# Kernel optimization log

Measured on AMD Instinct MI355X. Metric: run time of the kernel, lower is better.

Reference implementation:

```python
import jax, jax.numpy as jnp
import numpy as np

DIM = 1024
NUM_HEADS = 16
HEAD_DIM = DIM // NUM_HEADS  # 64
WINDOW = 256
SCALE = HEAD_DIM ** -0.5


def setup_inputs() -> dict:
    key = jax.random.key(0)
    ks = jax.random.split(key, 5)
    B, L = 4, 4096
    x = jax.random.normal(ks[0], (B, L, DIM), dtype=jnp.float32)
    # Linear weights stored torch-style as (out_features, in_features)
    q_w = jax.random.normal(ks[1], (DIM, DIM), dtype=jnp.float32) * (DIM ** -0.5)
    kv_w = jax.random.normal(ks[2], (2 * HEAD_DIM, DIM), dtype=jnp.float32) * (DIM ** -0.5)
    proj_w = jax.random.normal(ks[3], (DIM, DIM), dtype=jnp.float32) * (DIM ** -0.5)
    proj_b = jax.random.normal(ks[4], (DIM,), dtype=jnp.float32) * 0.01
    return {"x": x, "q_w": q_w, "kv_w": kv_w, "proj_w": proj_w, "proj_b": proj_b}


def reference(x, q_w, kv_w, proj_w, proj_b):
    B, L, D = x.shape
    H, hd, ws = NUM_HEADS, HEAD_DIM, WINDOW
    # MQA projections
    q = x @ q_w.T                                  # (B, L, D)
    kv = x @ kv_w.T                                # (B, L, 2*hd)
    k, v = kv[..., :hd], kv[..., hd:]              # (B, L, hd) single KV head
    q = q.reshape(B, L, H, hd).transpose(0, 2, 1, 3)  # (B, H, L, hd)
    # Pad sequence to a multiple of the window size (static at trace time)
    pad = (ws - L % ws) % ws
    Lp = L + pad
    if pad > 0:
        q = jnp.pad(q, ((0, 0), (0, 0), (0, pad), (0, 0)))
        k = jnp.pad(k, ((0, 0), (0, pad), (0, 0)))
        v = jnp.pad(v, ((0, 0), (0, pad), (0, 0)))
    n = Lp // ws
    qb = q.reshape(B, H, n, ws, hd)                # (B, H, n, w, d)
    kb = k.reshape(B, n, ws, hd)                   # (B, n, w, d) broadcast over heads
    vb = v.reshape(B, n, ws, hd)
    # Dense per-window attention with MQA-aware KV broadcast (no expand)
    attn = jnp.einsum('bhnwd,bnud->bhnwu', qb, kb) * SCALE
    attn = jax.nn.softmax(attn, axis=-1)
    out = jnp.einsum('bhnwu,bnud->bhnwd', attn, vb)  # (B, H, n, w, d)
    out = out.reshape(B, H, Lp, hd)[:, :, :L, :]
    out = out.transpose(0, 2, 1, 3).reshape(B, L, D)  # b h l d -> b l (h d)
    return out @ proj_w.T + proj_b
```

## Files before the change

### kernel.cpp

```cpp
#include <hip/hip_runtime.h>

typedef short bf16x8 __attribute__((ext_vector_type(8)));
typedef float f32x4 __attribute__((ext_vector_type(4)));

#define QSCALE 0.18033688011112042f

__device__ __forceinline__ unsigned short f2bf(float x) {
  unsigned int u = __float_as_uint(x);
  u = (u + 0x7FFFu + ((u >> 16) & 1u)) >> 16;
  return (unsigned short)u;
}

__device__ __forceinline__ unsigned pack_rn(float a, float b) {
  unsigned au = __float_as_uint(a) + 0x8000u;
  unsigned bu = __float_as_uint(b) + 0x8000u;
  return (bu & 0xFFFF0000u) | (au >> 16);
}

__device__ __forceinline__ void async16(const void* g, void* l) {
  typedef const __attribute__((address_space(1))) unsigned int* gp_t;
  typedef __attribute__((address_space(3))) unsigned int* lp_t;
  __builtin_amdgcn_global_load_lds((gp_t)g, (lp_t)l, 16, 0, 0);
}

union frag_u { bf16x8 f; unsigned int u[4]; };

__global__ void cast_bf16(const float* __restrict__ in, unsigned short* __restrict__ out, int n4) {
  int i = blockIdx.x * 256 + threadIdx.x;
  if (i >= n4) return;
  float4 v = ((const float4*)in)[i];
  ushort4 o;
  o.x = f2bf(v.x); o.y = f2bf(v.y); o.z = f2bf(v.z); o.w = f2bf(v.w);
  ((ushort4*)out)[i] = o;
}

__global__ void cast_w3(const float* __restrict__ qw, const float* __restrict__ kvw,
                        const float* __restrict__ pw, unsigned short* __restrict__ qwo,
                        unsigned short* __restrict__ kvwo, unsigned short* __restrict__ pwo) {
  int i = blockIdx.x * 256 + threadIdx.x;
  const float* src; unsigned short* dst; int j;
  if (i < 262144)      { src = qw;  dst = qwo;  j = i; }
  else if (i < 294912) { src = kvw; dst = kvwo; j = i - 262144; }
  else                 { src = pw;  dst = pwo;  j = i - 294912; }
  float4 v = ((const float4*)src)[j];
  ushort4 o;
  o.x = f2bf(v.x); o.y = f2bf(v.y); o.z = f2bf(v.z); o.w = f2bf(v.w);
  ((ushort4*)dst)[j] = o;
}

template<int MODE>
__global__ __launch_bounds__(512, 2) void gemm256(
    const unsigned short* __restrict__ A,
    const unsigned short* __restrict__ Bw,
    unsigned short* __restrict__ Cbf,
    float* __restrict__ Cf,
    const float* __restrict__ bias,
    const float oscale,
    int M, int N, int K)
{
  __shared__ unsigned short S[65536];
  const int t = threadIdx.x;
  const int lane = t & 63, wave = t >> 6;
  const int g = lane >> 4, r = lane & 15;
  const int wm = wave >> 2, wn = wave & 3;

  const int nby = N >> 8;
  const int cpx = gridDim.x >> 3;
  const int bid = blockIdx.x;
  const int swz = (bid & 7) * cpx + (bid >> 3);
  const long row0 = (long)(swz / nby) * 256;
  const long col0 = (long)(swz % nby) * 256;

  const int NT = K >> 6;

  auto stage = [&](const unsigned short* gsrc, long grow0, int kcol0, int region) {
#pragma unroll
    for (int i = 0; i < 2; ++i) {
      int o = (i * 512 + t) << 4;
      int row = o >> 7;
      int scol = (o & 127) ^ ((row & 7) << 4);
      async16(gsrc + (grow0 + row) * K + kcol0 + (scol >> 1),
              (char*)S + region + i * 8192 + wave * 1024);
    }
  };
  auto ldA = [&](int bo, int ar, int ks) {
    return *(const bf16x8*)((const char*)S + bo + ar * 128 +
                            ((ks * 64 + g * 16) ^ ((ar & 7) << 4)));
  };
  auto ldB = [&](int bo, int br, int ks) {
    return *(const bf16x8*)((const char*)S + bo + 32768 + br * 128 +
                            ((ks * 64 + g * 16) ^ ((br & 7) << 4)));
  };

  f32x4 acc[8][4] = {};
  bf16x8 aF[4][2], b01[2][2], b23[2][2];

  stage(A,  row0,       0, 0);
  stage(A,  row0 + 128, 0, 16384);
  stage(Bw, col0,       0, 32768);
  stage(Bw, col0 + 128, 0, 32768 + 16384);
  if (NT > 1) {
    stage(Bw, col0,       64, 65536 + 32768);
    stage(Bw, col0 + 128, 64, 65536 + 32768 + 16384);
    asm volatile("s_waitcnt vmcnt(4)" ::: "memory");
  } else {
    asm volatile("s_waitcnt vmcnt(0)" ::: "memory");
  }
  __builtin_amdgcn_s_barrier();

  for (int kt = 0; kt < NT; ++kt) {
    const int bo = (kt & 1) << 16;
    if (kt + 1 < NT) {
      stage(A, row0,       (kt + 1) * 64, bo ^ 65536);
      stage(A, row0 + 128, (kt + 1) * 64, (bo ^ 65536) + 16384);
    }
#pragma unroll
    for (int mf = 0; mf < 4; ++mf) {
      int ar = wm * 128 + mf * 16 + r;
      aF[mf][0] = ldA(bo, ar, 0); aF[mf][1] = ldA(bo, ar, 1);
    }
#pragma unroll
    for (int nf = 0; nf < 2; ++nf) {
      int br = wn * 64 + nf * 16 + r;
      b01[nf][0] = ldB(bo, br, 0); b01[nf][1] = ldB(bo, br, 1);
    }
#pragma unroll
    for (int nf = 0; nf < 2; ++nf) {
      int br = wn * 64 + (nf + 2) * 16 + r;
      b23[nf][0] = ldB(bo, br, 0); b23[nf][1] = ldB(bo, br, 1);
    }
    __builtin_amdgcn_s_setprio(1);
#pragma unroll
    for (int mf = 0; mf < 4; ++mf)
#pragma unroll
      for (int nf = 0; nf < 2; ++nf) {
        acc[mf][nf] = __builtin_amdgcn_mfma_f32_16x16x32_bf16(aF[mf][0], b01[nf][0], acc[mf][nf], 0, 0, 0);
        acc[mf][nf] = __builtin_amdgcn_mfma_f32_16x16x32_bf16(aF[mf][1], b01[nf][1], acc[mf][nf], 0, 0, 0);
        acc[mf][nf + 2] = __builtin_amdgcn_mfma_f32_16x16x32_bf16(aF[mf][0], b23[nf][0], acc[mf][nf + 2], 0, 0, 0);
        acc[mf][nf + 2] = __builtin_amdgcn_mfma_f32_16x16x32_bf16(aF[mf][1], b23[nf][1], acc[mf][nf + 2], 0, 0, 0);
      }
    __builtin_amdgcn_s_setprio(0);
    __builtin_amdgcn_s_barrier();
    if (kt + 2 < NT) {
      stage(Bw, col0,       (kt + 2) * 64, bo + 32768);
      stage(Bw, col0 + 128, (kt + 2) * 64, bo + 32768 + 16384);
    }
#pragma unroll
    for (int mf = 0; mf < 4; ++mf) {
      int ar = wm * 128 + (mf + 4) * 16 + r;
      aF[mf][0] = ldA(bo, ar, 0); aF[mf][1] = ldA(bo, ar, 1);
    }
    __builtin_amdgcn_s_setprio(1);
#pragma unroll
    for (int mf = 0; mf < 4; ++mf)
#pragma unroll
      for (int nf = 0; nf < 2; ++nf) {
        acc[mf + 4][nf] = __builtin_amdgcn_mfma_f32_16x16x32_bf16(aF[mf][0], b01[nf][0], acc[mf + 4][nf], 0, 0, 0);
        acc[mf + 4][nf] = __builtin_amdgcn_mfma_f32_16x16x32_bf16(aF[mf][1], b01[nf][1], acc[mf + 4][nf], 0, 0, 0);
        acc[mf + 4][nf + 2] = __builtin_amdgcn_mfma_f32_16x16x32_bf16(aF[mf][0], b23[nf][0], acc[mf + 4][nf + 2], 0, 0, 0);
        acc[mf + 4][nf + 2] = __builtin_amdgcn_mfma_f32_16x16x32_bf16(aF[mf][1], b23[nf][1], acc[mf + 4][nf + 2], 0, 0, 0);
      }
    __builtin_amdgcn_s_setprio(0);
    if (kt < NT - 2)      asm volatile("s_waitcnt vmcnt(4)" ::: "memory");
    else if (kt < NT - 1) asm volatile("s_waitcnt vmcnt(0)" ::: "memory");
    if (kt < NT - 1) __builtin_amdgcn_s_barrier();
  }

  if (MODE == 0) {
#pragma unroll
    for (int mf = 0; mf < 8; ++mf)
#pragma unroll
      for (int nf = 0; nf < 4; ++nf) {
        long rr = row0 + wm * 128 + mf * 16 + g * 4;
        long cc = col0 + wn * 64 + nf * 16 + r;
#pragma unroll
        for (int i = 0; i < 4; ++i)
          Cbf[(rr + i) * N + cc] = f2bf(acc[mf][nf][i] * oscale);
      }
  } else {
#pragma unroll
    for (int mf = 0; mf < 8; ++mf)
#pragma unroll
      for (int nf = 0; nf < 4; ++nf) {
        long rr = row0 + wm * 128 + mf * 16 + g * 4;
        long cc = col0 + wn * 64 + nf * 16 + r;
        float bb = bias[cc];
#pragma unroll
        for (int i = 0; i < 4; ++i)
          Cf[(rr + i) * N + cc] = acc[mf][nf][i] + bb;
      }
  }
}

__global__ __launch_bounds__(256) void gemm_kv(
    const unsigned short* __restrict__ A,
    const unsigned short* __restrict__ Bw,
    unsigned short* __restrict__ Kout,
    unsigned short* __restrict__ VTout,
    int M, int N, int K)
{
  __shared__ unsigned short As[128 * 64];
  __shared__ unsigned short Bs[128 * 64];
  const int t = threadIdx.x;
  const int lane = t & 63, wave = t >> 6;
  const int g = lane >> 4, r = lane & 15;
  const int wr = wave >> 1, wc = wave & 1;
  const long row0 = (long)blockIdx.x * 128;
  const long col0 = 0;

  f32x4 acc[4][4] = {};

  for (int kt = 0; kt < K; kt += 64) {
    __syncthreads();
#pragma unroll
    for (int i = 0; i < 4; ++i) {
      int o = (i * 256 + t) << 4;
      int arow = o >> 7;
      int scol = (o & 127) ^ ((arow & 7) << 4);
      async16(A + (row0 + arow) * K + kt + (scol >> 1), (char*)As + (i * 4096 + wave * 1024));
    }
#pragma unroll
    for (int i = 0; i < 4; ++i) {
      int o = (i * 256 + t) << 4;
      int brow = o >> 7;
      int scol = (o & 127) ^ ((brow & 7) << 4);
      async16(Bw + (col0 + brow) * K + kt + (scol >> 1), (char*)Bs + (i * 4096 + wave * 1024));
    }
    __syncthreads();
#pragma unroll
    for (int ks = 0; ks < 2; ++ks) {
      bf16x8 af[4], bfr[4];
#pragma unroll
      for (int rf = 0; rf < 4; ++rf) {
        int ar = wr * 64 + rf * 16 + r;
        af[rf] = *(const bf16x8*)((const char*)As + ar * 128 + ((ks * 64 + g * 16) ^ ((ar & 7) << 4)));
      }
#pragma unroll
      for (int cf = 0; cf < 4; ++cf) {
        int br = wc * 64 + cf * 16 + r;
        bfr[cf] = *(const bf16x8*)((const char*)Bs + br * 128 + ((ks * 64 + g * 16) ^ ((br & 7) << 4)));
      }
#pragma unroll
      for (int rf = 0; rf < 4; ++rf)
#pragma unroll
        for (int cf = 0; cf < 4; ++cf)
          acc[rf][cf] = __builtin_amdgcn_mfma_f32_16x16x32_bf16(af[rf], bfr[cf], acc[rf][cf], 0, 0, 0);
    }
  }

  if (wc == 0) {
#pragma unroll
    for (int rf = 0; rf < 4; ++rf)
#pragma unroll
      for (int cf = 0; cf < 4; ++cf) {
        long rr = row0 + wr * 64 + rf * 16 + g * 4;
        int cc = cf * 16 + r;
#pragma unroll
        for (int i = 0; i < 4; ++i)
          Kout[(rr + i) * 64 + cc] = f2bf(acc[rf][cf][i]);
      }
  } else {
#pragma unroll
    for (int rf = 0; rf < 4; ++rf)
#pragma unroll
      for (int cf = 0; cf < 4; ++cf) {
        long tok = row0 + wr * 64 + rf * 16 + g * 4;
        long w16 = tok >> 8;
        int kp = (int)(tok & 255);
        int hd = cf * 16 + r;
        ushort4 pk;
        pk.x = f2bf(acc[rf][cf][0]); pk.y = f2bf(acc[rf][cf][1]);
        pk.z = f2bf(acc[rf][cf][2]); pk.w = f2bf(acc[rf][cf][3]);
        *(ushort4*)(VTout + (w16 * 64 + hd) * 256 + kp) = pk;
      }
  }
}

__global__ __launch_bounds__(512, 2) void attn_win(
    const unsigned short* __restrict__ qb,
    const unsigned short* __restrict__ kb,
    const unsigned short* __restrict__ vt,
    unsigned short* __restrict__ ao)
{
  __shared__ unsigned short Ks[256 * 64];
  __shared__ unsigned short Vs[64 * 256];

  const int blk = blockIdx.x;
  const int hp = blk & 7;
  const int w16 = blk >> 3;
  const long tok0 = (long)w16 * 256;
  const int t = threadIdx.x;
  const int lane = t & 63, wave = t >> 6;
  const int g = lane >> 4, r = lane & 15;
  const int h = hp * 2 + (wave >> 2);
  const int qw = wave & 3;

#pragma unroll
  for (int i = 0; i < 4; ++i) {
    int o = (i * 512 + t) << 4;
    int row = o >> 7;
    int ph = ((row & 3) << 1) | ((row >> 3) & 1);
    int scol = (o & 127) ^ (ph << 4);
    async16(kb + (tok0 + row) * 64 + (scol >> 1), (char*)Ks + i * 8192 + wave * 1024);
  }
  const unsigned short* vbase = vt + (long)w16 * (64 * 256);
#pragma unroll
  for (int i = 0; i < 4; ++i) {
    int o = (i * 512 + t) << 4;
    int hd = o >> 9;
    int scol = (o & 511) ^ ((hd & 7) << 4);
    async16(vbase + (long)hd * 256 + (scol >> 1), (char*)Vs + i * 8192 + wave * 1024);
  }

  bf16x8 qf[4][2];
#pragma unroll
  for (int cq = 0; cq < 4; ++cq)
#pragma unroll
    for (int kh = 0; kh < 2; ++kh)
      qf[cq][kh] = *(const bf16x8*)(qb + (tok0 + qw * 64 + cq * 16 + r) * 1024 + h * 64 + kh * 32 + g * 8);

  f32x4 O[4][4] = {};
  float sp[4] = {0.f, 0.f, 0.f, 0.f};
  const int rsub = 8 * (r >> 2) + (r & 3);
  __syncthreads();

#pragma unroll
  for (int kc = 0; kc < 8; ++kc) {
    f32x4 sc[2][4] = {};
#pragma unroll
    for (int kr = 0; kr < 2; ++kr) {
      int kp = kc * 32 + kr * 4 + rsub;
      int ph = ((kp & 3) << 1) | ((kp >> 3) & 1);
      bf16x8 kf0 = *(const bf16x8*)((const char*)Ks + kp * 128 + ((g * 16) ^ (ph << 4)));
      bf16x8 kf1 = *(const bf16x8*)((const char*)Ks + kp * 128 + ((64 + g * 16) ^ (ph << 4)));
#pragma unroll
      for (int cq = 0; cq < 4; ++cq) {
        sc[kr][cq] = __builtin_amdgcn_mfma_f32_16x16x32_bf16(kf0, qf[cq][0], sc[kr][cq], 0, 0, 0);
        sc[kr][cq] = __builtin_amdgcn_mfma_f32_16x16x32_bf16(kf1, qf[cq][1], sc[kr][cq], 0, 0, 0);
      }
    }
    bf16x8 vf[4];
#pragma unroll
    for (int ch = 0; ch < 4; ++ch) {
      int hd = ch * 16 + r;
      vf[ch] = *(const bf16x8*)((const char*)Vs + hd * 512 + ((kc * 64 + g * 16) ^ ((hd & 7) << 4)));
    }
#pragma unroll
    for (int cq = 0; cq < 4; ++cq) {
#pragma unroll
      for (int kr = 0; kr < 2; ++kr)
#pragma unroll
        for (int i = 0; i < 4; ++i)
          sc[kr][cq][i] = __builtin_amdgcn_exp2f(sc[kr][cq][i]);
      sp[cq] += ((sc[0][cq][0] + sc[0][cq][1]) + (sc[0][cq][2] + sc[0][cq][3])) +
                ((sc[1][cq][0] + sc[1][cq][1]) + (sc[1][cq][2] + sc[1][cq][3]));
    }
#pragma unroll
    for (int rq = 0; rq < 4; ++rq) {
      frag_u pa;
      pa.u[0] = pack_rn(sc[0][rq][0], sc[0][rq][1]);
      pa.u[1] = pack_rn(sc[0][rq][2], sc[0][rq][3]);
      pa.u[2] = pack_rn(sc[1][rq][0], sc[1][rq][1]);
      pa.u[3] = pack_rn(sc[1][rq][2], sc[1][rq][3]);
#pragma unroll
      for (int ch = 0; ch < 4; ++ch)
        O[rq][ch] = __builtin_amdgcn_mfma_f32_16x16x32_bf16(pa.f, vf[ch], O[rq][ch], 0, 0, 0);
    }
  }
  float inv[4];
#pragma unroll
  for (int cq = 0; cq < 4; ++cq) {
    float s = sp[cq];
    s += __shfl_xor(s, 16);
    s += __shfl_xor(s, 32);
    inv[cq] = 1.0f / s;
  }
#pragma unroll
  for (int rq = 0; rq < 4; ++rq)
#pragma unroll
    for (int i = 0; i < 4; ++i) {
      float w = __shfl(inv[rq], g * 4 + i);
      long tokr = tok0 + qw * 64 + rq * 16 + g * 4 + i;
#pragma unroll
      for (int ch = 0; ch < 4; ++ch)
        ao[tokr * 1024 + h * 64 + ch * 16 + r] = f2bf(O[rq][ch][i] * w);
    }
}

extern "C" void kernel_launch(void* const* d_in, const int* in_sizes, int n_in,
                              void* d_out, int out_size, void* d_ws, size_t ws_size,
                              hipStream_t stream) {
  const float* x      = (const float*)d_in[0];
  const float* q_w    = (const float*)d_in[1];
  const float* kv_w   = (const float*)d_in[2];
  const float* proj_w = (const float*)d_in[3];
  const float* proj_b = (const float*)d_in[4];

  char* ws = (char*)d_ws;
  unsigned short* x_bf   = (unsigned short*)(ws + 0);
  unsigned short* q_bf   = (unsigned short*)(ws + 33554432);
  unsigned short* ao_bf  = (unsigned short*)(ws + 67108864);
  unsigned short* qw_bf  = (unsigned short*)(ws + 100663296);
  unsigned short* pw_bf  = (unsigned short*)(ws + 102760448);
  unsigned short* kvw_bf = (unsigned short*)(ws + 104857600);
  unsigned short* k_bf   = (unsigned short*)(ws + 105119744);
  unsigned short* vt_bf  = (unsigned short*)(ws + 107216896);
  if (ws_size < 109314048) return;

  cast_bf16<<<16384, 256, 0, stream>>>(x, x_bf, 4194304);
  cast_w3<<<2176, 256, 0, stream>>>(q_w, kv_w, proj_w, qw_bf, kvw_bf, pw_bf);

  gemm256<0><<<256, 512, 0, stream>>>(x_bf, qw_bf, q_bf, nullptr, nullptr, QSCALE, 16384, 1024, 1024);
  gemm_kv<<<128, 256, 0, stream>>>(x_bf, kvw_bf, k_bf, vt_bf, 16384, 128, 1024);
  attn_win<<<512, 512, 0, stream>>>(q_bf, k_bf, vt_bf, ao_bf);
  gemm256<1><<<256, 512, 0, stream>>>(ao_bf, pw_bf, nullptr, (float*)d_out, proj_b, 1.0f, 16384, 1024, 1024);
}
```

Baseline: 148.5 us.

## Fuse fp32-to-bf16 cast of x into Q and KV projection GEMM loads

Removes the standalone cast kernel for x and has both the Q-projection GEMM and the KV GEMM read fp32 x directly. Each thread loads float4s into registers, packs them to bf16 and writes them swizzled into shared memory, replacing the async global-to-LDS copy for the A operand. This saves a full write and re-read of the 32 MB bf16 copy of x and one launch. In exchange the GEMMs read twice as many A bytes, and x is now read twice in fp32, once per GEMM. The register staging also adds VGPR pressure and extra waitcnt/barrier handling in the pipelined loop.

```diff
diff --git a/kernel.cpp b/kernel.cpp
--- a/kernel.cpp
+++ b/kernel.cpp
@@ -2,6 +2,7 @@
 
 typedef short bf16x8 __attribute__((ext_vector_type(8)));
 typedef float f32x4 __attribute__((ext_vector_type(4)));
+typedef unsigned int u32x4 __attribute__((ext_vector_type(4)));
 
 #define QSCALE 0.18033688011112042f
 
@@ -24,15 +25,6 @@
 }
 
 union frag_u { bf16x8 f; unsigned int u[4]; };
-
-__global__ void cast_bf16(const float* __restrict__ in, unsigned short* __restrict__ out, int n4) {
-  int i = blockIdx.x * 256 + threadIdx.x;
-  if (i >= n4) return;
-  float4 v = ((const float4*)in)[i];
-  ushort4 o;
-  o.x = f2bf(v.x); o.y = f2bf(v.y); o.z = f2bf(v.z); o.w = f2bf(v.w);
-  ((ushort4*)out)[i] = o;
-}
 
 __global__ void cast_w3(const float* __restrict__ qw, const float* __restrict__ kvw,
                         const float* __restrict__ pw, unsigned short* __restrict__ qwo,
@@ -50,7 +42,7 @@
 
 template<int MODE>
 __global__ __launch_bounds__(512, 2) void gemm256(
-    const unsigned short* __restrict__ A,
+    const void* __restrict__ Asrc,
     const unsigned short* __restrict__ Bw,
     unsigned short* __restrict__ Cbf,
     float* __restrict__ Cf,
@@ -73,15 +65,32 @@
 
   const int NT = K >> 6;
 
-  auto stage = [&](const unsigned short* gsrc, long grow0, int kcol0, int region) {
-#pragma unroll
-    for (int i = 0; i < 2; ++i) {
-      int o = (i * 512 + t) << 4;
-      int row = o >> 7;
-      int scol = (o & 127) ^ ((row & 7) << 4);
-      async16(gsrc + (grow0 + row) * K + kcol0 + (scol >> 1),
-              (char*)S + region + i * 8192 + wave * 1024);
-    }
+  const float* Af = (const float*)Asrc;
+  const unsigned short* Ab = (const unsigned short*)Asrc;
+
+  auto stageB = [&](int kt, int region) {
+#pragma unroll
+    for (int h = 0; h < 2; ++h)
+#pragma unroll
+      for (int i = 0; i < 2; ++i) {
+        int o = (i * 512 + t) << 4;
+        int row = o >> 7;
+        int scol = (o & 127) ^ ((row & 7) << 4);
+        async16(Bw + (col0 + h * 128 + row) * K + kt * 64 + (scol >> 1),
+                (char*)S + region + h * 16384 + i * 8192 + wave * 1024);
+      }
+  };
+  auto stageAb = [&](int kt, int region) {
+#pragma unroll
+    for (int h = 0; h < 2; ++h)
+#pragma unroll
+      for (int i = 0; i < 2; ++i) {
+        int o = (i * 512 + t) << 4;
+        int row = o >> 7;
+        int scol = (o & 127) ^ ((row & 7) << 4);
+        async16(Ab + (row0 + h * 128 + row) * K + kt * 64 + (scol >> 1),
+                (char*)S + region + h * 16384 + i * 8192 + wave * 1024);
+      }
   };
   auto ldA = [&](int bo, int ar, int ks) {
     return *(const bf16x8*)((const char*)S + bo + ar * 128 +
@@ -92,27 +101,63 @@
                             ((ks * 64 + g * 16) ^ ((br & 7) << 4)));
   };
 
+  float4 areg[8];
+  const int arow = t >> 1, ac0 = (t & 1) * 32;
+  auto issueA = [&](int kt) {
+    const float4* src = (const float4*)(Af + (row0 + arow) * (long)K + kt * 64 + ac0);
+#pragma unroll
+    for (int i = 0; i < 8; ++i) areg[i] = src[i];
+  };
+  auto writeA = [&](int kt) {
+    char* base = (char*)S + ((kt & 1) << 16) + arow * 128;
+#pragma unroll
+    for (int w = 0; w < 4; ++w) {
+      u32x4 u;
+      u[0] = pack_rn(areg[2 * w].x, areg[2 * w].y);
+      u[1] = pack_rn(areg[2 * w].z, areg[2 * w].w);
+      u[2] = pack_rn(areg[2 * w + 1].x, areg[2 * w + 1].y);
+      u[3] = pack_rn(areg[2 * w + 1].z, areg[2 * w + 1].w);
+      int bc = (ac0 * 2 + w * 16) ^ ((arow & 7) << 4);
+      *(u32x4*)(base + bc) = u;
+    }
+  };
+
   f32x4 acc[8][4] = {};
   bf16x8 aF[4][2], b01[2][2], b23[2][2];
 
-  stage(A,  row0,       0, 0);
-  stage(A,  row0 + 128, 0, 16384);
-  stage(Bw, col0,       0, 32768);
-  stage(Bw, col0 + 128, 0, 32768 + 16384);
-  if (NT > 1) {
-    stage(Bw, col0,       64, 65536 + 32768);
-    stage(Bw, col0 + 128, 64, 65536 + 32768 + 16384);
+  if (MODE == 0) {
+    issueA(0);
+    stageB(0, 32768);
     asm volatile("s_waitcnt vmcnt(4)" ::: "memory");
+    writeA(0);
+    if (NT > 1) {
+      issueA(1);
+      stageB(1, 65536 + 32768);
+      asm volatile("s_waitcnt vmcnt(4)" ::: "memory");
+      writeA(1);
+    } else {
+      asm volatile("s_waitcnt vmcnt(0)" ::: "memory");
+    }
+    asm volatile("s_waitcnt lgkmcnt(0)" ::: "memory");
+    __builtin_amdgcn_s_barrier();
   } else {
-    asm volatile("s_waitcnt vmcnt(0)" ::: "memory");
-  }
-  __builtin_amdgcn_s_barrier();
+    stageAb(0, 0);
+    stageB(0, 32768);
+    if (NT > 1) {
+      stageB(1, 65536 + 32768);
+      asm volatile("s_waitcnt vmcnt(4)" ::: "memory");
+    } else {
+      asm volatile("s_waitcnt vmcnt(0)" ::: "memory");
+    }
+    __builtin_amdgcn_s_barrier();
+  }
 
   for (int kt = 0; kt < NT; ++kt) {
     const int bo = (kt & 1) << 16;
-    if (kt + 1 < NT) {
-      stage(A, row0,       (kt + 1) * 64, bo ^ 65536);
-      stage(A, row0 + 128, (kt + 1) * 64, (bo ^ 65536) + 16384);
+    if (MODE == 0) {
+      if (kt + 1 < NT) issueA(kt + 1);
+    } else {
+      if (kt + 1 < NT) stageAb(kt + 1, bo ^ 65536);
     }
 #pragma unroll
     for (int mf = 0; mf < 4; ++mf) {
@@ -141,14 +186,18 @@
       }
     __builtin_amdgcn_s_setprio(0);
     __builtin_amdgcn_s_barrier();
-    if (kt + 2 < NT) {
-      stage(Bw, col0,       (kt + 2) * 64, bo + 32768);
-      stage(Bw, col0 + 128, (kt + 2) * 64, bo + 32768 + 16384);
-    }
+    if (kt + 2 < NT) stageB(kt + 2, bo + 32768);
 #pragma unroll
     for (int mf = 0; mf < 4; ++mf) {
       int ar = wm * 128 + (mf + 4) * 16 + r;
       aF[mf][0] = ldA(bo, ar, 0); aF[mf][1] = ldA(bo, ar, 1);
+    }
+    if (MODE == 0) {
+      if (kt + 1 < NT) {
+        if (kt + 2 < NT) asm volatile("s_waitcnt vmcnt(4)" ::: "memory");
+        else             asm volatile("s_waitcnt vmcnt(0)" ::: "memory");
+        writeA(kt + 1);
+      }
     }
     __builtin_amdgcn_s_setprio(1);
 #pragma unroll
@@ -161,9 +210,14 @@
         acc[mf + 4][nf + 2] = __builtin_amdgcn_mfma_f32_16x16x32_bf16(aF[mf][1], b23[nf][1], acc[mf + 4][nf + 2], 0, 0, 0);
       }
     __builtin_amdgcn_s_setprio(0);
-    if (kt < NT - 2)      asm volatile("s_waitcnt vmcnt(4)" ::: "memory");
-    else if (kt < NT - 1) asm volatile("s_waitcnt vmcnt(0)" ::: "memory");
-    if (kt < NT - 1) __builtin_amdgcn_s_barrier();
+    if (MODE == 1) {
+      if (kt < NT - 2)      asm volatile("s_waitcnt vmcnt(4)" ::: "memory");
+      else if (kt < NT - 1) asm volatile("s_waitcnt vmcnt(0)" ::: "memory");
+    }
+    if (kt < NT - 1) {
+      asm volatile("s_waitcnt lgkmcnt(0)" ::: "memory");
+      __builtin_amdgcn_s_barrier();
+    }
   }
 
   if (MODE == 0) {
@@ -193,7 +247,7 @@
 }
 
 __global__ __launch_bounds__(256) void gemm_kv(
-    const unsigned short* __restrict__ A,
+    const float* __restrict__ Af,
     const unsigned short* __restrict__ Bw,
     unsigned short* __restrict__ Kout,
     unsigned short* __restrict__ VTout,
@@ -206,25 +260,32 @@
   const int g = lane >> 4, r = lane & 15;
   const int wr = wave >> 1, wc = wave & 1;
   const long row0 = (long)blockIdx.x * 128;
-  const long col0 = 0;
+  const int arow = t >> 1, ac0 = (t & 1) * 32;
 
   f32x4 acc[4][4] = {};
 
   for (int kt = 0; kt < K; kt += 64) {
     __syncthreads();
-#pragma unroll
-    for (int i = 0; i < 4; ++i) {
-      int o = (i * 256 + t) << 4;
-      int arow = o >> 7;
-      int scol = (o & 127) ^ ((arow & 7) << 4);
-      async16(A + (row0 + arow) * K + kt + (scol >> 1), (char*)As + (i * 4096 + wave * 1024));
-    }
+    float4 av[8];
+    const float4* src = (const float4*)(Af + (row0 + arow) * (long)K + kt + ac0);
+#pragma unroll
+    for (int i = 0; i < 8; ++i) av[i] = src[i];
 #pragma unroll
     for (int i = 0; i < 4; ++i) {
       int o = (i * 256 + t) << 4;
       int brow = o >> 7;
       int scol = (o & 127) ^ ((brow & 7) << 4);
-      async16(Bw + (col0 + brow) * K + kt + (scol >> 1), (char*)Bs + (i * 4096 + wave * 1024));
+      async16(Bw + brow * K + kt + (scol >> 1), (char*)Bs + (i * 4096 + wave * 1024));
+    }
+#pragma unroll
+    for (int w = 0; w < 4; ++w) {
+      u32x4 u;
+      u[0] = pack_rn(av[2 * w].x, av[2 * w].y);
+      u[1] = pack_rn(av[2 * w].z, av[2 * w].w);
+      u[2] = pack_rn(av[2 * w + 1].x, av[2 * w + 1].y);
+      u[3] = pack_rn(av[2 * w + 1].z, av[2 * w + 1].w);
+      int bc = (ac0 * 2 + w * 16) ^ ((arow & 7) << 4);
+      *(u32x4*)((char*)As + arow * 128 + bc) = u;
     }
     __syncthreads();
 #pragma unroll
@@ -397,7 +458,6 @@
   const float* proj_b = (const float*)d_in[4];
 
   char* ws = (char*)d_ws;
-  unsigned short* x_bf   = (unsigned short*)(ws + 0);
   unsigned short* q_bf   = (unsigned short*)(ws + 33554432);
   unsigned short* ao_bf  = (unsigned short*)(ws + 67108864);
   unsigned short* qw_bf  = (unsigned short*)(ws + 100663296);
@@ -407,11 +467,10 @@
   unsigned short* vt_bf  = (unsigned short*)(ws + 107216896);
   if (ws_size < 109314048) return;
 
-  cast_bf16<<<16384, 256, 0, stream>>>(x, x_bf, 4194304);
   cast_w3<<<2176, 256, 0, stream>>>(q_w, kv_w, proj_w, qw_bf, kvw_bf, pw_bf);
 
-  gemm256<0><<<256, 512, 0, stream>>>(x_bf, qw_bf, q_bf, nullptr, nullptr, QSCALE, 16384, 1024, 1024);
-  gemm_kv<<<128, 256, 0, stream>>>(x_bf, kvw_bf, k_bf, vt_bf, 16384, 128, 1024);
+  gemm256<0><<<256, 512, 0, stream>>>(x, qw_bf, q_bf, nullptr, nullptr, QSCALE, 16384, 1024, 1024);
+  gemm_kv<<<128, 256, 0, stream>>>(x, kvw_bf, k_bf, vt_bf, 16384, 128, 1024);
   attn_win<<<512, 512, 0, stream>>>(q_bf, k_bf, vt_bf, ao_bf);
   gemm256<1><<<256, 512, 0, stream>>>(ao_bf, pw_bf, nullptr, (float*)d_out, proj_b, 1.0f, 16384, 1024, 1024);
 }
```

Measured after the change: 212.1 us. +42.9%, slower.
